# Kernel optimization log

Hardware: AMD Instinct MI355X
Metric: run time of the kernel (lower is better)

Reference implementation:

```python
import jax, jax.numpy as jnp
import numpy as np

N_HEAD = 16

def setup_inputs() -> dict:
    key = jax.random.key(0)
    ks = jax.random.split(key, 5)
    B, S, D = 4, 2048, 1024
    return {
        "string": jax.random.normal(ks[0], (B, S, D), dtype=jnp.float32),
        "string_len": jax.random.randint(ks[1], (B,), 1, S + 1),
        "Wqkv": jax.random.normal(ks[2], (D, 3 * D), dtype=jnp.float32) * 0.02,
        "bqkv": jnp.zeros((3 * D,), dtype=jnp.float32),
        "Wo": jax.random.normal(ks[3], (D, D), dtype=jnp.float32) * 0.02,
        "bo": jnp.zeros((D,), dtype=jnp.float32),
    }


def reference(string, string_len, Wqkv, bqkv, Wo, bo):
    B, S, D = string.shape
    H = N_HEAD
    hd = D // H
    x = string @ Wqkv + bqkv                      # [B,S,3D]
    q, k, v = jnp.split(x, 3, axis=-1)
    # split heads -> [B,H,S,hd]
    q = q.reshape(B, S, H, hd).transpose(0, 2, 1, 3)
    k = k.reshape(B, S, H, hd).transpose(0, 2, 1, 3)
    v = v.reshape(B, S, H, hd).transpose(0, 2, 1, 3)
    w = jnp.einsum('bhqd,bhkd->bhqk', q, k) / jnp.sqrt(jnp.float32(hd))
    causal = jnp.tril(jnp.ones((S, S), dtype=bool))  # [S,S]
    w = jnp.where(causal[None, None], w, jnp.float32(-1e9))
    w = jax.nn.softmax(w, axis=-1)
    a = jnp.einsum('bhqk,bhkd->bhqd', w, v)       # [B,H,S,hd]
    a = a.transpose(0, 2, 1, 3).reshape(B, S, D)  # merge heads
    a = a @ Wo + bo
    return a, string_len
```

## Files before the change

### kernel.cpp

```cpp
#include <hip/hip_runtime.h>
#include <hip/hip_fp8.h>
#include <stdint.h>

typedef __attribute__((ext_vector_type(8))) short bf16x8;
typedef __attribute__((ext_vector_type(4))) float f32x4;
typedef __attribute__((ext_vector_type(16))) float f32x16;
typedef __attribute__((ext_vector_type(4))) unsigned short u16x4;

static constexpr int Bn = 4, Sn = 2048, Dn = 1024, Hn = 16, HD = 64;
static constexpr int Mrows = Bn * Sn;
static constexpr int D3 = 3 * Dn;

__device__ __forceinline__ unsigned short f2bf(float f) {
  unsigned int u = __float_as_uint(f);
  u += 0x7FFF + ((u >> 16) & 1);
  return (unsigned short)(u >> 16);
}

__device__ __forceinline__ unsigned char f2fp8(float f) {
  __hip_fp8_e4m3 v(f);
  return (unsigned char)v.__x;
}

__device__ __forceinline__ void gload16(const void* gptr, void* lptr) {
  __builtin_amdgcn_global_load_lds(
      (__attribute__((address_space(1))) void*)gptr,
      (__attribute__((address_space(3))) void*)lptr, 16, 0, 0);
}

__device__ __forceinline__ int swz8(int r) { return (r ^ (r >> 3)) & 7; }

__device__ __forceinline__ float vexp2(float x) {
#if __has_builtin(__builtin_amdgcn_exp2f)
  return __builtin_amdgcn_exp2f(x);
#else
  return exp2f(x);
#endif
}

__device__ __forceinline__ unsigned cvtpk(float lo, float hi) {
  unsigned r;
  asm("v_cvt_pk_bf16_f32 %0, %1, %2" : "=v"(r) : "v"(lo), "v"(hi));
  return r;
}

__device__ __forceinline__ float lanepull(float v, int srclane) {
  return __int_as_float(__builtin_amdgcn_ds_bpermute(srclane * 4, __float_as_int(v)));
}

__global__ void cvt_f32_fp8(const float* __restrict__ in,
                            unsigned char* __restrict__ out, int n) {
  int i = (blockIdx.x * blockDim.x + threadIdx.x) * 4;
  if (i < n) {
    const float4 v = *(const float4*)(in + i);
    uchar4 o;
    o.x = f2fp8(v.x); o.y = f2fp8(v.y); o.z = f2fp8(v.z); o.w = f2fp8(v.w);
    *(uchar4*)(out + i) = o;
  }
}

__global__ void transpose_cvt_fp8(const float* __restrict__ W,
                                  unsigned char* __restrict__ Wt, int K, int N) {
  __shared__ float tile[32][33];
  const int n0 = blockIdx.x * 32, k0 = blockIdx.y * 32;
  const int tx = threadIdx.x, ty = threadIdx.y;
  #pragma unroll
  for (int j = 0; j < 4; j++)
    tile[ty + 8 * j][tx] = W[(size_t)(k0 + ty + 8 * j) * N + n0 + tx];
  __syncthreads();
  #pragma unroll
  for (int j = 0; j < 4; j++)
    Wt[(size_t)(n0 + ty + 8 * j) * K + k0 + tx] = f2fp8(tile[tx][ty + 8 * j] * 64.0f);
}

template<bool BF16_OUT>
__global__ __launch_bounds__(512, 1)
void gemm_fp8(const unsigned char* __restrict__ A,
              const unsigned char* __restrict__ Bt,
              const float* __restrict__ bias,
              void* __restrict__ Cout, int Nt, int Kt) {
  __shared__ __align__(128) unsigned char smem[98304];
  const int tid = threadIdx.x;
  const int w = tid >> 6, lane = tid & 63;
  const int wm = w >> 2, wn = w & 3;
  const int lrow = lane & 15, lk = lane >> 4;
  const long brow = (long)blockIdx.x * 128;
  const long bcol = (long)blockIdx.y * 256;

  const int srow = tid >> 3;
  const int sslot = tid & 7;

  auto stage = [&](int k0, unsigned char* buf) {
    unsigned char* Ab = buf;
    unsigned char* Bb = buf + 16384;
    #pragma unroll
    for (int i = 0; i < 2; i++) {
      const int r = srow + 64 * i;
      gload16(A + (size_t)(brow + r) * Kt + k0 + ((sslot ^ swz8(r)) * 16),
              Ab + w * 1024 + i * 8192);
    }
    #pragma unroll
    for (int i = 0; i < 4; i++) {
      const int r = srow + 64 * i;
      gload16(Bt + (size_t)(bcol + r) * Kt + k0 + ((sslot ^ swz8(r)) * 16),
              Bb + w * 1024 + i * 8192);
    }
  };

  f32x4 acc[4][4] = {};

  stage(0, smem);

  const int ntile = Kt >> 7;
  for (int t = 0; t < ntile; t++) {
    const int cur = t & 1;
    unsigned char* Ab = smem + cur * 49152;
    unsigned char* Bb = Ab + 16384;

    __builtin_amdgcn_s_barrier();
    if (t + 1 < ntile) {
      stage((t + 1) << 7, smem + (cur ^ 1) * 49152);
      asm volatile("s_waitcnt vmcnt(6)");
    } else {
      asm volatile("s_waitcnt vmcnt(0)");
    }
    __builtin_amdgcn_sched_barrier(0);
    __builtin_amdgcn_s_barrier();

    const int sub = (lk & 1) * 8;
    #pragma unroll
    for (int kk = 0; kk < 4; kk++) {
      const int s16 = kk * 2 + (lk >> 1);
      long av[4], bv[4];
      #pragma unroll
      for (int mt = 0; mt < 4; mt++) {
        const int r = wm * 64 + mt * 16 + lrow;
        av[mt] = *(const long*)(Ab + r * 128 + (((s16 ^ swz8(r)) << 4) + sub));
      }
      #pragma unroll
      for (int nt = 0; nt < 4; nt++) {
        const int r = wn * 64 + nt * 16 + lrow;
        bv[nt] = *(const long*)(Bb + r * 128 + (((s16 ^ swz8(r)) << 4) + sub));
      }
      __builtin_amdgcn_s_setprio(1);
      #pragma unroll
      for (int mt = 0; mt < 4; mt++)
        #pragma unroll
        for (int nt = 0; nt < 4; nt++)
          acc[mt][nt] = __builtin_amdgcn_mfma_f32_16x16x32_fp8_fp8(av[mt], bv[nt], acc[mt][nt], 0, 0, 0);
      __builtin_amdgcn_s_setprio(0);
    }
  }

  #pragma unroll
  for (int nt = 0; nt < 4; nt++) {
    const long col = bcol + wn * 64 + nt * 16 + lrow;
    const float bv2 = bias[col];
    #pragma unroll
    for (int mt = 0; mt < 4; mt++) {
      #pragma unroll
      for (int rr = 0; rr < 4; rr++) {
        const long row = brow + wm * 64 + mt * 16 + lk * 4 + rr;
        const float v = acc[mt][nt][rr] * 0.015625f + bv2;
        if (BF16_OUT)
          ((unsigned short*)Cout)[row * Nt + col] = f2bf(v);
        else
          ((float*)Cout)[row * Nt + col] = v;
      }
    }
  }
}

__global__ __launch_bounds__(512, 1)
void attn_pair(const unsigned short* __restrict__ QKV,
               unsigned char* __restrict__ Out) {
  __shared__ __align__(128) unsigned char smem[65536];
  const int tid  = threadIdx.x;
  const int w    = tid >> 6;
  const int lane = tid & 63;
  const int li = lane & 31, hi = lane >> 5;
  const int bh = blockIdx.x;
  const int b  = bh >> 4, h = bh & 15;
  const int p  = blockIdx.y;
  const int wqh = (7 - p) * 256 + w * 32;
  const int wql = p * 256 + w * 32;

  const float cexp = 0.18033688011112042f;

  bf16x8 qfh[4], qfl[4];
  {
    const unsigned short* qp = QKV + (size_t)(b * Sn + wqh + li) * D3 + h * HD + hi * 8;
    #pragma unroll
    for (int ks = 0; ks < 4; ks++) qfh[ks] = *(const bf16x8*)(qp + ks * 16);
  }
  {
    const unsigned short* qp = QKV + (size_t)(b * Sn + wql + li) * D3 + h * HD + hi * 8;
    #pragma unroll
    for (int ks = 0; ks < 4; ks++) qfl[ks] = *(const bf16x8*)(qp + ks * 16);
  }

  f32x16 o0h = {}, o1h = {}, o0l = {}, o1l = {};
  float mh = -3.0e38f, lsh = 0.f, ml = -3.0e38f, lsl = 0.f;

  auto kstage = [&](int kb, unsigned char* Kb) {
    #pragma unroll
    for (int i = 0; i < 2; i++) {
      const int r    = w * 16 + i * 8 + (lane >> 3);
      const int slot = (lane & 7) ^ swz8(r);
      gload16(QKV + (size_t)(b * Sn + kb + r) * D3 + Dn + h * HD + slot * 8,
              Kb + w * 2048 + i * 1024);
    }
  };
  const int vkv8 = tid >> 3;
  const int vd0  = (tid & 7) * 8;
  auto vload = [&](int kb, int i) -> bf16x8 {
    return *(const bf16x8*)(QKV + (size_t)(b * Sn + kb + i * 64 + vkv8) * D3 + 2 * Dn + h * HD + vd0);
  };
  auto vwrite = [&](bf16x8 vv, int i, unsigned char* Vb) {
    const int kv = i * 64 + vkv8;
    #pragma unroll
    for (int jj = 0; jj < 8; jj++) {
      const int d  = vd0 + jj;
      const int vs = (d ^ (d >> 3)) & 15;
      *(unsigned short*)(Vb + d * 256 + (((kv >> 3) ^ vs) << 4) + (kv & 7) * 2) = (unsigned short)vv[jj];
    }
  };

  auto substep = [&](int s, int kb, const unsigned char* Kb, const unsigned char* Vb,
                     int wqX, bf16x8 (&qf)[4], f32x16& o0, f32x16& o1,
                     float& m, float& ls) {
    const int qrowX = wqX + li;
    f32x16 s0 = {}, s1 = {};
    const int r0 = s * 64 + li, r1 = s * 64 + 32 + li;
    __builtin_amdgcn_s_setprio(1);
    #pragma unroll
    for (int ks = 0; ks < 4; ks++) {
      const int slot = ks * 2 + hi;
      const bf16x8 k0 = *(const bf16x8*)(Kb + r0 * 128 + ((slot ^ swz8(r0)) * 16));
      const bf16x8 k1 = *(const bf16x8*)(Kb + r1 * 128 + ((slot ^ swz8(r1)) * 16));
      s0 = __builtin_amdgcn_mfma_f32_32x32x16_bf16(k0, qf[ks], s0, 0, 0, 0);
      s1 = __builtin_amdgcn_mfma_f32_32x32x16_bf16(k1, qf[ks], s1, 0, 0, 0);
    }
    __builtin_amdgcn_s_setprio(0);
    const int kbase = kb + s * 64;
    if (kbase + 63 > wqX) {
      #pragma unroll
      for (int r = 0; r < 16; r++) {
        const int kvl = (r & 3) + 8 * (r >> 2) + 4 * hi;
        if (kbase + kvl > qrowX)      s0[r] = -3.0e38f;
        if (kbase + 32 + kvl > qrowX) s1[r] = -3.0e38f;
      }
    }
    float t8[8];
    #pragma unroll
    for (int r = 0; r < 8; r++)
      t8[r] = fmaxf(fmaxf(s0[r], s0[r + 8]), fmaxf(s1[r], s1[r + 8]));
    float tmax = fmaxf(fmaxf(fmaxf(t8[0], t8[1]), fmaxf(t8[2], t8[3])),
                       fmaxf(fmaxf(t8[4], t8[5]), fmaxf(t8[6], t8[7])));
    tmax = fmaxf(tmax, __shfl_xor(tmax, 32));
    if (__any(tmax > m + 44.0f)) {
      const float mn   = fmaxf(m, tmax);
      const float corr = vexp2((m - mn) * cexp);
      m = mn;
      ls *= corr;
      #pragma unroll
      for (int r = 0; r < 16; r++) {
        const float cr = lanepull(corr, (r & 3) + 8 * (r >> 2) + 4 * hi);
        o0[r] *= cr; o1[r] *= cr;
      }
    }
    const float mc = m * cexp;
    f32x16 p0, p1;
    float psa = 0.f, psb = 0.f, psc = 0.f, psd = 0.f;
    #pragma unroll
    for (int r = 0; r < 16; r += 4) {
      p0[r] = vexp2(fmaf(s0[r], cexp, -mc));         psa += p0[r];
      p0[r + 1] = vexp2(fmaf(s0[r + 1], cexp, -mc)); psb += p0[r + 1];
      p0[r + 2] = vexp2(fmaf(s0[r + 2], cexp, -mc)); psc += p0[r + 2];
      p0[r + 3] = vexp2(fmaf(s0[r + 3], cexp, -mc)); psd += p0[r + 3];
    }
    #pragma unroll
    for (int r = 0; r < 16; r += 4) {
      p1[r] = vexp2(fmaf(s1[r], cexp, -mc));         psa += p1[r];
      p1[r + 1] = vexp2(fmaf(s1[r + 1], cexp, -mc)); psb += p1[r + 1];
      p1[r + 2] = vexp2(fmaf(s1[r + 2], cexp, -mc)); psc += p1[r + 2];
      p1[r + 3] = vexp2(fmaf(s1[r + 3], cexp, -mc)); psd += p1[r + 3];
    }
    ls += (psa + psb) + (psc + psd);

    auto mk_pa = [&](const f32x16& pp, int base) -> bf16x8 {
      const unsigned a0 = cvtpk(pp[base + 0], pp[base + 1]);
      const unsigned a1 = cvtpk(pp[base + 2], pp[base + 3]);
      const unsigned b0 = cvtpk(pp[base + 4], pp[base + 5]);
      const unsigned b1 = cvtpk(pp[base + 6], pp[base + 7]);
      const unsigned xa0 = __shfl_xor(a0, 32), xa1 = __shfl_xor(a1, 32);
      const unsigned xb0 = __shfl_xor(b0, 32), xb1 = __shfl_xor(b1, 32);
      union { unsigned u[4]; bf16x8 v; } pu;
      pu.u[0] = hi ? xb0 : a0;
      pu.u[1] = hi ? xb1 : a1;
      pu.u[2] = hi ? b0  : xa0;
      pu.u[3] = hi ? b1  : xa1;
      return pu.v;
    };
    bf16x8 pa[4];
    pa[0] = mk_pa(p0, 0); pa[1] = mk_pa(p0, 8);
    pa[2] = mk_pa(p1, 0); pa[3] = mk_pa(p1, 8);

    const int vs0 = (li ^ (li >> 3)) & 15;
    const int vs1 = ((32 + li) ^ ((32 + li) >> 3)) & 15;
    __builtin_amdgcn_s_setprio(1);
    #pragma unroll
    for (int k16 = 0; k16 < 4; k16++) {
      const int slot = s * 8 + k16 * 2 + hi;
      const bf16x8 vb0 = *(const bf16x8*)(Vb + li * 256 + ((slot ^ vs0) << 4));
      const bf16x8 vb1 = *(const bf16x8*)(Vb + (32 + li) * 256 + ((slot ^ vs1) << 4));
      o0 = __builtin_amdgcn_mfma_f32_32x32x16_bf16(pa[k16], vb0, o0, 0, 0, 0);
      o1 = __builtin_amdgcn_mfma_f32_32x32x16_bf16(pa[k16], vb1, o1, 0, 0, 0);
    }
    __builtin_amdgcn_s_setprio(0);
  };

  kstage(0, smem);
  {
    bf16x8 va = vload(0, 0), vb = vload(0, 1);
    vwrite(va, 0, smem + 16384);
    vwrite(vb, 1, smem + 16384);
  }
  asm volatile("s_waitcnt lgkmcnt(0)");
  __builtin_amdgcn_sched_barrier(0);

  const int nt = 16 - 2 * p;
  for (int t = 0; t < nt; t++) {
    const int kb  = t << 7;
    const int cur = t & 1;
    unsigned char* Kb = smem + cur * 32768;
    unsigned char* Vb = Kb + 16384;
    const bool pre = (t + 1 < nt);
    bf16x8 vna, vnb;

    __builtin_amdgcn_s_barrier();
    if (pre) {
      kstage(kb + 128, smem + (cur ^ 1) * 32768);
      vna = vload(kb + 128, 0);
      vnb = vload(kb + 128, 1);
    }

    if (kb <= wqh + 31) {
      substep(0, kb, Kb, Vb, wqh, qfh, o0h, o1h, mh, lsh);
      if (kb + 64 <= wqh + 31) substep(1, kb, Kb, Vb, wqh, qfh, o0h, o1h, mh, lsh);
    }
    if (kb <= wql + 31) {
      substep(0, kb, Kb, Vb, wql, qfl, o0l, o1l, ml, lsl);
      if (kb + 64 <= wql + 31) substep(1, kb, Kb, Vb, wql, qfl, o0l, o1l, ml, lsl);
    }

    if (pre) {
      unsigned char* Vn = smem + (cur ^ 1) * 32768 + 16384;
      vwrite(vna, 0, Vn);
      vwrite(vnb, 1, Vn);
    }
    asm volatile("s_waitcnt lgkmcnt(0)");
    __builtin_amdgcn_sched_barrier(0);
  }

  {
    const float lt = lsh + __shfl_xor(lsh, 32);
    const float rl = __builtin_amdgcn_rcpf(lt);
    #pragma unroll
    for (int r = 0; r < 16; r++) {
      const int q = (r & 3) + 8 * (r >> 2) + 4 * hi;
      const float rr = lanepull(rl, q);
      unsigned char* op = Out + (size_t)(b * Sn + wqh + q) * Dn + h * HD;
      op[li]      = f2fp8(o0h[r] * rr);
      op[32 + li] = f2fp8(o1h[r] * rr);
    }
  }
  {
    const float lt = lsl + __shfl_xor(lsl, 32);
    const float rl = __builtin_amdgcn_rcpf(lt);
    #pragma unroll
    for (int r = 0; r < 16; r++) {
      const int q = (r & 3) + 8 * (r >> 2) + 4 * hi;
      const float rr = lanepull(rl, q);
      unsigned char* op = Out + (size_t)(b * Sn + wql + q) * Dn + h * HD;
      op[li]      = f2fp8(o0l[r] * rr);
      op[32 + li] = f2fp8(o1l[r] * rr);
    }
  }
}

__global__ void copy_len(const int* __restrict__ slen, float* __restrict__ dst, int n) {
  const int i = threadIdx.x;
  if (i < n) dst[i] = (float)slen[i];
}

extern "C" void kernel_launch(void* const* d_in, const int* in_sizes, int n_in,
                              void* d_out, int out_size, void* d_ws, size_t ws_size,
                              hipStream_t stream) {
  const float* X    = (const float*)d_in[0];
  const int*   slen = (const int*)d_in[1];
  const float* Wqkv = (const float*)d_in[2];
  const float* bqkv = (const float*)d_in[3];
  const float* Wo   = (const float*)d_in[4];
  const float* bo   = (const float*)d_in[5];
  float* out = (float*)d_out;

  char* ws = (char*)d_ws;
  unsigned char*  Xf8   = (unsigned char*)ws;
  unsigned char*  Wtq8  = (unsigned char*)(ws + 16777216);
  unsigned char*  Wto8  = (unsigned char*)(ws + 16777216 + 6291456);
  unsigned short* QKVb  = (unsigned short*)(ws + 16777216 + 6291456 + 2097152);
  unsigned char*  Attnb = (unsigned char*)ws;

  cvt_f32_fp8<<<dim3(8192), dim3(256), 0, stream>>>(X, Xf8, Mrows * Dn);
  transpose_cvt_fp8<<<dim3(96, 32), dim3(32, 8), 0, stream>>>(Wqkv, Wtq8, Dn, D3);
  transpose_cvt_fp8<<<dim3(32, 32), dim3(32, 8), 0, stream>>>(Wo, Wto8, Dn, Dn);

  gemm_fp8<true><<<dim3(64, 12), dim3(512), 0, stream>>>(Xf8, Wtq8, bqkv, (void*)QKVb, D3, Dn);
  attn_pair<<<dim3(64, 4), dim3(512), 0, stream>>>(QKVb, Attnb);
  gemm_fp8<false><<<dim3(64, 4), dim3(512), 0, stream>>>(Attnb, Wto8, bo, d_out, Dn, Dn);
  copy_len<<<dim3(1), dim3(64), 0, stream>>>(slen, out + (size_t)Mrows * Dn, Bn);
}
```

Measured before the change: 152.0 us.

## Replace paired causal attention blocks with longest-first single query-tile blocks

The attention kernel drops the scheme that paired a high and a low 256-row query tile per 512-thread block. Instead it launches 1024 blocks of 256 threads, each handling one 128-row query tile, ordered longest-first so the largest causal workloads are scheduled before the short ones. Shared memory shrinks to 32KB with a single K/V buffer, which lets up to 4 blocks share a CU. In exchange the cross-iteration double-buffered prefetch is gone: every iteration loads K/V synchronously between two barriers, and K/V tiles are reloaded by more blocks overall.

```diff
diff --git a/kernel.cpp b/kernel.cpp
--- a/kernel.cpp
+++ b/kernel.cpp
@@ -171,65 +171,59 @@
   }
 }
 
-__global__ __launch_bounds__(512, 1)
-void attn_pair(const unsigned short* __restrict__ QKV,
-               unsigned char* __restrict__ Out) {
-  __shared__ __align__(128) unsigned char smem[65536];
+__global__ __launch_bounds__(256, 4)
+void attn_lpt(const unsigned short* __restrict__ QKV,
+              unsigned char* __restrict__ Out) {
+  __shared__ __align__(128) unsigned char smem[32768];
   const int tid  = threadIdx.x;
   const int w    = tid >> 6;
   const int lane = tid & 63;
   const int li = lane & 31, hi = lane >> 5;
   const int bh = blockIdx.x;
   const int b  = bh >> 4, h = bh & 15;
-  const int p  = blockIdx.y;
-  const int wqh = (7 - p) * 256 + w * 32;
-  const int wql = p * 256 + w * 32;
+  const int m  = 15 - (int)blockIdx.y;
+  const int wq = m * 128 + w * 32;
+  const int qrow = wq + li;
 
   const float cexp = 0.18033688011112042f;
 
-  bf16x8 qfh[4], qfl[4];
+  bf16x8 qf[4];
   {
-    const unsigned short* qp = QKV + (size_t)(b * Sn + wqh + li) * D3 + h * HD + hi * 8;
-    #pragma unroll
-    for (int ks = 0; ks < 4; ks++) qfh[ks] = *(const bf16x8*)(qp + ks * 16);
-  }
-  {
-    const unsigned short* qp = QKV + (size_t)(b * Sn + wql + li) * D3 + h * HD + hi * 8;
-    #pragma unroll
-    for (int ks = 0; ks < 4; ks++) qfl[ks] = *(const bf16x8*)(qp + ks * 16);
-  }
-
-  f32x16 o0h = {}, o1h = {}, o0l = {}, o1l = {};
-  float mh = -3.0e38f, lsh = 0.f, ml = -3.0e38f, lsl = 0.f;
-
-  auto kstage = [&](int kb, unsigned char* Kb) {
-    #pragma unroll
-    for (int i = 0; i < 2; i++) {
-      const int r    = w * 16 + i * 8 + (lane >> 3);
+    const unsigned short* qp = QKV + (size_t)(b * Sn + qrow) * D3 + h * HD + hi * 8;
+    #pragma unroll
+    for (int ks = 0; ks < 4; ks++) qf[ks] = *(const bf16x8*)(qp + ks * 16);
+  }
+
+  f32x16 o0 = {}, o1 = {};
+  float mm = -3.0e38f, ls = 0.f;
+
+  unsigned char* Kb = smem;
+  unsigned char* Vb = smem + 16384;
+
+  auto kstage = [&](int kb) {
+    #pragma unroll
+    for (int i = 0; i < 4; i++) {
+      const int r    = i * 32 + w * 8 + (lane >> 3);
       const int slot = (lane & 7) ^ swz8(r);
       gload16(QKV + (size_t)(b * Sn + kb + r) * D3 + Dn + h * HD + slot * 8,
-              Kb + w * 2048 + i * 1024);
-    }
-  };
-  const int vkv8 = tid >> 3;
-  const int vd0  = (tid & 7) * 8;
-  auto vload = [&](int kb, int i) -> bf16x8 {
-    return *(const bf16x8*)(QKV + (size_t)(b * Sn + kb + i * 64 + vkv8) * D3 + 2 * Dn + h * HD + vd0);
-  };
-  auto vwrite = [&](bf16x8 vv, int i, unsigned char* Vb) {
-    const int kv = i * 64 + vkv8;
-    #pragma unroll
-    for (int jj = 0; jj < 8; jj++) {
-      const int d  = vd0 + jj;
+              Kb + i * 4096 + w * 1024);
+    }
+  };
+  const int vkv = tid >> 1;
+  const int vd0 = (tid & 1) * 32;
+  auto vload = [&](int kb, int jj) -> bf16x8 {
+    return *(const bf16x8*)(QKV + (size_t)(b * Sn + kb + vkv) * D3 + 2 * Dn + h * HD + vd0 + jj * 8);
+  };
+  auto vwrite = [&](bf16x8 vv, int jj) {
+    #pragma unroll
+    for (int e = 0; e < 8; e++) {
+      const int d  = vd0 + jj * 8 + e;
       const int vs = (d ^ (d >> 3)) & 15;
-      *(unsigned short*)(Vb + d * 256 + (((kv >> 3) ^ vs) << 4) + (kv & 7) * 2) = (unsigned short)vv[jj];
-    }
-  };
-
-  auto substep = [&](int s, int kb, const unsigned char* Kb, const unsigned char* Vb,
-                     int wqX, bf16x8 (&qf)[4], f32x16& o0, f32x16& o1,
-                     float& m, float& ls) {
-    const int qrowX = wqX + li;
+      *(unsigned short*)(Vb + d * 256 + (((vkv >> 3) ^ vs) << 4) + (vkv & 7) * 2) = (unsigned short)vv[e];
+    }
+  };
+
+  auto substep = [&](int s, int kb) {
     f32x16 s0 = {}, s1 = {};
     const int r0 = s * 64 + li, r1 = s * 64 + 32 + li;
     __builtin_amdgcn_s_setprio(1);
@@ -243,12 +237,12 @@
     }
     __builtin_amdgcn_s_setprio(0);
     const int kbase = kb + s * 64;
-    if (kbase + 63 > wqX) {
+    if (kbase + 63 > wq) {
       #pragma unroll
       for (int r = 0; r < 16; r++) {
         const int kvl = (r & 3) + 8 * (r >> 2) + 4 * hi;
-        if (kbase + kvl > qrowX)      s0[r] = -3.0e38f;
-        if (kbase + 32 + kvl > qrowX) s1[r] = -3.0e38f;
+        if (kbase + kvl > qrow)      s0[r] = -3.0e38f;
+        if (kbase + 32 + kvl > qrow) s1[r] = -3.0e38f;
       }
     }
     float t8[8];
@@ -258,10 +252,10 @@
     float tmax = fmaxf(fmaxf(fmaxf(t8[0], t8[1]), fmaxf(t8[2], t8[3])),
                        fmaxf(fmaxf(t8[4], t8[5]), fmaxf(t8[6], t8[7])));
     tmax = fmaxf(tmax, __shfl_xor(tmax, 32));
-    if (__any(tmax > m + 44.0f)) {
-      const float mn   = fmaxf(m, tmax);
-      const float corr = vexp2((m - mn) * cexp);
-      m = mn;
+    if (__any(tmax > mm + 44.0f)) {
+      const float mn   = fmaxf(mm, tmax);
+      const float corr = vexp2((mm - mn) * cexp);
+      mm = mn;
       ls *= corr;
       #pragma unroll
       for (int r = 0; r < 16; r++) {
@@ -269,7 +263,7 @@
         o0[r] *= cr; o1[r] *= cr;
       }
     }
-    const float mc = m * cexp;
+    const float mc = mm * cexp;
     f32x16 p0, p1;
     float psa = 0.f, psb = 0.f, psc = 0.f, psd = 0.f;
     #pragma unroll
@@ -320,72 +314,31 @@
     __builtin_amdgcn_s_setprio(0);
   };
 
-  kstage(0, smem);
-  {
-    bf16x8 va = vload(0, 0), vb = vload(0, 1);
-    vwrite(va, 0, smem + 16384);
-    vwrite(vb, 1, smem + 16384);
-  }
-  asm volatile("s_waitcnt lgkmcnt(0)");
-  __builtin_amdgcn_sched_barrier(0);
-
-  const int nt = 16 - 2 * p;
-  for (int t = 0; t < nt; t++) {
-    const int kb  = t << 7;
-    const int cur = t & 1;
-    unsigned char* Kb = smem + cur * 32768;
-    unsigned char* Vb = Kb + 16384;
-    const bool pre = (t + 1 < nt);
-    bf16x8 vna, vnb;
-
+  for (int t = 0; t <= m; t++) {
+    const int kb = t << 7;
     __builtin_amdgcn_s_barrier();
-    if (pre) {
-      kstage(kb + 128, smem + (cur ^ 1) * 32768);
-      vna = vload(kb + 128, 0);
-      vnb = vload(kb + 128, 1);
-    }
-
-    if (kb <= wqh + 31) {
-      substep(0, kb, Kb, Vb, wqh, qfh, o0h, o1h, mh, lsh);
-      if (kb + 64 <= wqh + 31) substep(1, kb, Kb, Vb, wqh, qfh, o0h, o1h, mh, lsh);
-    }
-    if (kb <= wql + 31) {
-      substep(0, kb, Kb, Vb, wql, qfl, o0l, o1l, ml, lsl);
-      if (kb + 64 <= wql + 31) substep(1, kb, Kb, Vb, wql, qfl, o0l, o1l, ml, lsl);
-    }
-
-    if (pre) {
-      unsigned char* Vn = smem + (cur ^ 1) * 32768 + 16384;
-      vwrite(vna, 0, Vn);
-      vwrite(vnb, 1, Vn);
-    }
-    asm volatile("s_waitcnt lgkmcnt(0)");
+    kstage(kb);
+    {
+      bf16x8 v0 = vload(kb, 0), v1 = vload(kb, 1), v2 = vload(kb, 2), v3 = vload(kb, 3);
+      vwrite(v0, 0); vwrite(v1, 1); vwrite(v2, 2); vwrite(v3, 3);
+    }
+    asm volatile("s_waitcnt vmcnt(0) lgkmcnt(0)");
     __builtin_amdgcn_sched_barrier(0);
-  }
-
-  {
-    const float lt = lsh + __shfl_xor(lsh, 32);
-    const float rl = __builtin_amdgcn_rcpf(lt);
-    #pragma unroll
-    for (int r = 0; r < 16; r++) {
-      const int q = (r & 3) + 8 * (r >> 2) + 4 * hi;
-      const float rr = lanepull(rl, q);
-      unsigned char* op = Out + (size_t)(b * Sn + wqh + q) * Dn + h * HD;
-      op[li]      = f2fp8(o0h[r] * rr);
-      op[32 + li] = f2fp8(o1h[r] * rr);
-    }
-  }
-  {
-    const float lt = lsl + __shfl_xor(lsl, 32);
-    const float rl = __builtin_amdgcn_rcpf(lt);
-    #pragma unroll
-    for (int r = 0; r < 16; r++) {
-      const int q = (r & 3) + 8 * (r >> 2) + 4 * hi;
-      const float rr = lanepull(rl, q);
-      unsigned char* op = Out + (size_t)(b * Sn + wql + q) * Dn + h * HD;
-      op[li]      = f2fp8(o0l[r] * rr);
-      op[32 + li] = f2fp8(o1l[r] * rr);
-    }
+    __builtin_amdgcn_s_barrier();
+
+    substep(0, kb);
+    if (kb + 64 <= wq + 31) substep(1, kb);
+  }
+
+  const float lt = ls + __shfl_xor(ls, 32);
+  const float rl = __builtin_amdgcn_rcpf(lt);
+  #pragma unroll
+  for (int r = 0; r < 16; r++) {
+    const int q = (r & 3) + 8 * (r >> 2) + 4 * hi;
+    const float rr = lanepull(rl, q);
+    unsigned char* op = Out + (size_t)(b * Sn + wq + q) * Dn + h * HD;
+    op[li]      = f2fp8(o0[r] * rr);
+    op[32 + li] = f2fp8(o1[r] * rr);
   }
 }
 
@@ -417,7 +370,7 @@
   transpose_cvt_fp8<<<dim3(32, 32), dim3(32, 8), 0, stream>>>(Wo, Wto8, Dn, Dn);
 
   gemm_fp8<true><<<dim3(64, 12), dim3(512), 0, stream>>>(Xf8, Wtq8, bqkv, (void*)QKVb, D3, Dn);
-  attn_pair<<<dim3(64, 4), dim3(512), 0, stream>>>(QKVb, Attnb);
+  attn_lpt<<<dim3(64, 16), dim3(256), 0, stream>>>(QKVb, Attnb);
   gemm_fp8<false><<<dim3(64, 4), dim3(512), 0, stream>>>(Attnb, Wto8, bo, d_out, Dn, Dn);
   copy_len<<<dim3(1), dim3(64), 0, stream>>>(slen, out + (size_t)Mrows * Dn, Bn);
 }
```

After: 295.1 us. 1.94x slower.
